# Kernel optimization log

Measured on AMD Instinct MI355X. Metric: run time of the kernel, lower is better.

Reference implementation:

```python
import jax, jax.numpy as jnp
import numpy as np

H, NOPE, ROPE, VD, KV_LORA, HID = 16, 128, 64, 128, 512, 2048
QK = NOPE + ROPE
SCALE = QK ** -0.5
EPS = 1e-5


def _rope(x, freqs):
    # x: [b, t, h, ROPE]; freqs: [t, ROPE//2] angles. Complex-pair rotation.
    cos = jnp.cos(freqs)[None, :, None, :]
    sin = jnp.sin(freqs)[None, :, None, :]
    xr = x.reshape(x.shape[:-1] + (ROPE // 2, 2))
    x1, x2 = xr[..., 0], xr[..., 1]
    o1 = x1 * cos - x2 * sin
    o2 = x1 * sin + x2 * cos
    return jnp.stack([o1, o2], axis=-1).reshape(x.shape)


def _layernorm(x, g, b):
    mu = jnp.mean(x, axis=-1, keepdims=True)
    var = jnp.var(x, axis=-1, keepdims=True)
    return (x - mu) * jax.lax.rsqrt(var + EPS) * g + b


def setup_inputs() -> dict:
    key = jax.random.key(0)
    ks = jax.random.split(key, 6)
    b, t = 2, 2048

    def xavier(k, shape):
        fan_in, fan_out = shape
        lim = np.sqrt(6.0 / (fan_in + fan_out))
        return jax.random.uniform(k, shape, jnp.float32, -lim, lim)

    hidden_states = jax.random.normal(ks[0], (b, t, HID), jnp.float32)
    # rope angles: theta_i = 10000^(-2i/ROPE), angle[p,i] = p * theta_i
    inv_freq = 1.0 / (10000.0 ** (np.arange(0, ROPE, 2, dtype=np.float32) / ROPE))
    freqs = jnp.asarray(np.arange(t, dtype=np.float32)[:, None] * inv_freq[None, :])
    # causal additive mask broadcastable to [b,t,s,h]
    causal = jnp.where(jnp.arange(t)[None, :] <= jnp.arange(t)[:, None], 0.0, -1e9)
    attention_mask = causal.astype(jnp.float32)[None, :, :, None]
    return {
        "hidden_states": hidden_states,
        "freqs": freqs,
        "attention_mask": attention_mask,
        "Wq": xavier(ks[1], (HID, H * QK)),
        "Wkv_a": xavier(ks[2], (HID, KV_LORA + ROPE)),
        "kv_gamma": jnp.ones((KV_LORA,), jnp.float32),
        "kv_beta": jnp.zeros((KV_LORA,), jnp.float32),
        "Wkv_b": xavier(ks[3], (KV_LORA, H * (NOPE + VD))),
        "Wout": xavier(ks[4], (H * VD, HID)),
    }


def reference(hidden_states, freqs, attention_mask, Wq, Wkv_a, kv_gamma, kv_beta, Wkv_b, Wout):
    b, t, _ = hidden_states.shape
    # Q projection -> [b,t,H,QK], split nope/rope, rotate rope part
    q = (hidden_states @ Wq).reshape(b, t, H, QK)
    q_nope, q_rope = q[..., :NOPE], q[..., NOPE:]
    q_rope = _rope(q_rope, freqs)
    # compressed KV latent + shared rope key
    kv = hidden_states @ Wkv_a                      # [b,t,KV_LORA+ROPE]
    kv_lat, k_rope = kv[..., :KV_LORA], kv[..., KV_LORA:]
    k_rope = _rope(k_rope[:, :, None, :], freqs)    # [b,t,1,ROPE]
    kv_lat = _layernorm(kv_lat, kv_gamma, kv_beta)
    kvb = (kv_lat @ Wkv_b).reshape(b, t, H, NOPE + VD)
    k_nope, v = kvb[..., :NOPE], kvb[..., NOPE:]
    k = jnp.concatenate([k_nope, jnp.broadcast_to(k_rope, (b, t, H, ROPE))], axis=-1)
    q = jnp.concatenate([q_nope, q_rope], axis=-1)
    # scores [b,t,s,h]; NOTE: source applies softmax over dim=-1 == HEAD axis (faithful)
    scores = jnp.einsum("bthd,bshd->btsh", q, k) * SCALE + attention_mask
    weights = jax.nn.softmax(scores.astype(jnp.float32), axis=-1).astype(q.dtype)
    attn = jnp.einsum("btsh,bshd->bthd", weights, v).reshape(b, t, H * VD)
    return attn @ Wout
```

## Files before the change

### kernel.cpp

```cpp
#include <hip/hip_runtime.h>

typedef unsigned short u16;
typedef short bf16x8 __attribute__((ext_vector_type(8)));
typedef float f32x4 __attribute__((ext_vector_type(4)));
typedef float f32x16 __attribute__((ext_vector_type(16)));
typedef unsigned short u16x8 __attribute__((ext_vector_type(8)));
typedef unsigned short u16x4 __attribute__((ext_vector_type(4)));

#define GLOBAL_AS __attribute__((address_space(1)))
#define LDS_AS __attribute__((address_space(3)))
#define DEVINL __device__ __forceinline__

#define BATCH 2
#define TSEQ 2048
#define NHEAD 16
#define QK 192
#define VD 128
#define HID 2048
#define MROWS 4096
#define SCALE_QK 0.07216878364870323f

DEVINL float b2f(u16 u) { union { unsigned i; float f; } x; x.i = ((unsigned)u) << 16; return x.f; }
DEVINL u16 f2b(float f) {
    union { float f; unsigned u; } x; x.f = f;
    unsigned r = x.u + 0x7fffu + ((x.u >> 16) & 1u);
    return (u16)(r >> 16);
}
DEVINL void gload_lds16(const u16* g, u16* l) {
    __builtin_amdgcn_global_load_lds((const GLOBAL_AS unsigned*)g, (LDS_AS unsigned*)l, 16, 0, 0);
}
DEVINL unsigned pk2(float a, float b) {
    unsigned d;
    asm("v_cvt_pk_bf16_f32 %0, %1, %2" : "=v"(d) : "v"(a), "v"(b));
    return d;
}


__global__ void cvt_bf16x8(const float* __restrict__ in, u16* __restrict__ out, int n8) {
    int i = blockIdx.x * 256 + threadIdx.x;
    if (i < n8) {
        const float4* p = (const float4*)(in + (size_t)i * 8);
        float4 x = p[0], y = p[1];
        u16x8 o;
        o[0] = f2b(x.x); o[1] = f2b(x.y); o[2] = f2b(x.z); o[3] = f2b(x.w);
        o[4] = f2b(y.x); o[5] = f2b(y.y); o[6] = f2b(y.z); o[7] = f2b(y.w);
        *(u16x8*)(out + (size_t)i * 8) = o;
    }
}

__global__ void rope_tab_k(const float* __restrict__ freqs, float2* __restrict__ tab) {
    int i = blockIdx.x * 256 + threadIdx.x;
    float f = freqs[i], s, c;
    sincosf(f, &s, &c);
    tab[i] = make_float2(c, s);
}

__global__ void transpose_cvt(const float* __restrict__ in, u16* __restrict__ out,
                              int R, int C, int Cpad) {
    __shared__ float tile[32][33];
    int c0 = blockIdx.x * 32, r0 = blockIdx.y * 32;
    int tx = threadIdx.x, ty = threadIdx.y;
#pragma unroll
    for (int j = 0; j < 4; j++) {
        int r = r0 + ty + j * 8, c = c0 + tx;
        tile[ty + j * 8][tx] = (c < C) ? in[(size_t)r * C + c] : 0.f;
    }
    __syncthreads();
#pragma unroll
    for (int j = 0; j < 4; j++) {
        int oc = c0 + ty + j * 8;
        int orr = r0 + tx;
        if (oc < Cpad) out[(size_t)oc * R + orr] = f2b(tile[tx][ty + j * 8]);
    }
}

template<int MODE>
__global__ __launch_bounds__(256)
void gemm_bt(const u16* __restrict__ A, const u16* __restrict__ BT, int Kdim,
             void* __restrict__ out0, void* __restrict__ out1, void* __restrict__ out2,
             const float2* __restrict__ tab) {
    __shared__ __align__(16) u16 As[128 * 32];
    __shared__ __align__(16) u16 Bs[128 * 32];
    const int tid = threadIdx.x, lane = tid & 63, wave = tid >> 6;
    const int m0 = blockIdx.x * 128, n0 = blockIdx.y * 128;
    const int wr = wave >> 1, wc = wave & 1;

    f32x4 acc[4][4];
#pragma unroll
    for (int i = 0; i < 4; i++)
#pragma unroll
        for (int j = 0; j < 4; j++) acc[i][j] = f32x4{0.f, 0.f, 0.f, 0.f};

    const int e0 = (wave * 2 + 0) * 512 + lane * 8;
    const int e1 = (wave * 2 + 1) * 512 + lane * 8;
    const u16* gA0 = A + (size_t)(m0 + (e0 >> 5)) * Kdim + (e0 & 31);
    const u16* gA1 = A + (size_t)(m0 + (e1 >> 5)) * Kdim + (e1 & 31);
    const u16* gB0 = BT + (size_t)(n0 + (e0 >> 5)) * Kdim + (e0 & 31);
    const u16* gB1 = BT + (size_t)(n0 + (e1 >> 5)) * Kdim + (e1 & 31);
    u16* lA0 = &As[(wave * 2 + 0) * 512];
    u16* lA1 = &As[(wave * 2 + 1) * 512];
    u16* lB0 = &Bs[(wave * 2 + 0) * 512];
    u16* lB1 = &Bs[(wave * 2 + 1) * 512];

    const int arow = lane & 15, koff = (lane >> 4) * 8;

    for (int k0 = 0; k0 < Kdim; k0 += 32) {
        gload_lds16(gA0, lA0); gload_lds16(gA1, lA1);
        gload_lds16(gB0, lB0); gload_lds16(gB1, lB1);
        gA0 += 32; gA1 += 32; gB0 += 32; gB1 += 32;
        asm volatile("s_waitcnt vmcnt(0)" ::: "memory");
        __syncthreads();
        bf16x8 af[4], bfr[4];
#pragma unroll
        for (int i = 0; i < 4; i++)
            af[i] = *(const bf16x8*)&As[(wr * 64 + i * 16 + arow) * 32 + koff];
#pragma unroll
        for (int j = 0; j < 4; j++)
            bfr[j] = *(const bf16x8*)&Bs[(wc * 64 + j * 16 + arow) * 32 + koff];
#pragma unroll
        for (int i = 0; i < 4; i++)
#pragma unroll
            for (int j = 0; j < 4; j++)
                acc[i][j] = __builtin_amdgcn_mfma_f32_16x16x32_bf16(af[i], bfr[j], acc[i][j], 0, 0, 0);
        __syncthreads();
    }

#pragma unroll
    for (int i = 0; i < 4; i++)
#pragma unroll
        for (int j = 0; j < 4; j++)
#pragma unroll
            for (int r = 0; r < 4; r++) {
                int row = m0 + wr * 64 + i * 16 + (lane >> 4) * 4 + r;
                int col = n0 + wc * 64 + j * 16 + (lane & 15);
                float v = acc[i][j][r];
                if constexpr (MODE == 0) {
                    int h = col / 192, d = col % 192;
                    int b = row >> 11, t = row & 2047;
                    float vv = v;
                    float pv = __shfl_xor(v, 1);
                    if (d >= 128) {
                        float2 cs = tab[t * 32 + ((d - 128) >> 1)];
                        vv = v * cs.x + pv * ((lane & 1) ? cs.y : -cs.y);
                    }
                    ((u16*)out0)[((size_t)(b * 16 + h) * 2048 + t) * 192 + d] = f2b(vv);
                } else if constexpr (MODE == 1) {
                    ((float*)out0)[(size_t)row * 640 + col] = v;
                } else if constexpr (MODE == 2) {
                    int h = col >> 8, d = col & 255;
                    int b = row >> 11, t = row & 2047;
                    size_t base = (size_t)(b * 16 + h) * 2048 + t;
                    if (d < 128) ((u16*)out0)[base * 192 + d] = f2b(v);
                    else {
                        u16 bv = f2b(v);
                        ((u16*)out1)[base * 128 + (d - 128)] = bv;
                        ((u16*)out2)[((size_t)(b * 16 + h) * 128 + (d - 128)) * 2048 + t] = bv;
                    }
                } else {
                    ((float*)out0)[(size_t)row * 2048 + col] = v;
                }
            }
}

__global__ __launch_bounds__(256)
void ln_krope(const float* __restrict__ kvf, const float* __restrict__ gamma,
              const float* __restrict__ beta, const float2* __restrict__ tab,
              u16* __restrict__ kvlat, u16* __restrict__ kbuf) {
    int row = blockIdx.x, tid = threadIdx.x;
    const float* x = kvf + (size_t)row * 640;
    float v0 = x[tid], v1 = x[tid + 256];
    float s = v0 + v1, sq = v0 * v0 + v1 * v1;
#pragma unroll
    for (int off = 1; off < 64; off <<= 1) { s += __shfl_xor(s, off); sq += __shfl_xor(sq, off); }
    __shared__ float ssum[4], ssq[4];
    if ((tid & 63) == 0) { ssum[tid >> 6] = s; ssq[tid >> 6] = sq; }
    __syncthreads();
    s = ssum[0] + ssum[1] + ssum[2] + ssum[3];
    sq = ssq[0] + ssq[1] + ssq[2] + ssq[3];
    float mu = s * (1.f / 512.f);
    float var = sq * (1.f / 512.f) - mu * mu;
    float rs = rsqrtf(var + 1e-5f);
    kvlat[(size_t)row * 512 + tid] = f2b((v0 - mu) * rs * gamma[tid] + beta[tid]);
    kvlat[(size_t)row * 512 + tid + 256] = f2b((v1 - mu) * rs * gamma[tid + 256] + beta[tid + 256]);
    if (tid < 32) {
        int t = row & 2047, b = row >> 11;
        float x1 = x[512 + 2 * tid], x2 = x[512 + 2 * tid + 1];
        float2 cs = tab[t * 32 + tid];
        u16 u1 = f2b(x1 * cs.x - x2 * cs.y), u2 = f2b(x1 * cs.y + x2 * cs.x);
        for (int h = 0; h < 16; ++h) {
            size_t base = ((size_t)(b * 16 + h) * 2048 + t) * 192 + 128 + 2 * tid;
            kbuf[base] = u1; kbuf[base + 1] = u2;
        }
    }
}

__global__ void suff1(const u16* __restrict__ vbuf, float* __restrict__ psum) {
    int bh = blockIdx.x, c = blockIdx.y, d = threadIdx.x;
    float s = 0.f;
    const u16* vp = vbuf + ((size_t)bh * 2048 + c * 128) * 128 + d;
    for (int tt = 0; tt < 128; ++tt) s += b2f(vp[(size_t)tt * 128]);
    psum[((size_t)bh * 16 + c) * 128 + d] = s;
}
__global__ void suff2(const float* __restrict__ psum, float* __restrict__ csuf) {
    int bh = blockIdx.x, d = threadIdx.x;
    float run = 0.f;
    for (int c = 15; c >= 0; --c) {
        csuf[((size_t)bh * 16 + c) * 128 + d] = run;
        run += psum[((size_t)bh * 16 + c) * 128 + d];
    }
}
__global__ void suff3(const u16* __restrict__ vbuf, const float* __restrict__ csuf,
                      u16* __restrict__ attnb) {
    int bh = blockIdx.x, c = blockIdx.y, d = threadIdx.x;
    int b = bh >> 4, h = bh & 15;
    float run = csuf[((size_t)bh * 16 + c) * 128 + d];
    for (int tt = 127; tt >= 0; --tt) {
        int t = c * 128 + tt;
        attnb[((size_t)b * 2048 + t) * 2048 + h * 128 + d] = f2b(run * 0.0625f);
        run += b2f(vbuf[((size_t)bh * 2048 + t) * 128 + d]);
    }
}

__global__ __launch_bounds__(256, 3)
void z_kernel(const u16* __restrict__ qbuf, const u16* __restrict__ kbuf,
              u16* __restrict__ ztb) {
    __shared__ __align__(16) u16 Ks[2 * 12288];
    const int tid = threadIdx.x, lane = tid & 63, wave = tid >> 6;
    const int hi = lane >> 5, l31 = lane & 31;
    const int tgrp = wave & 1, sblk = wave >> 1;
    int id = blockIdx.x;
    int b = id & 1, p = id >> 1;
    int tT = 0;
    for (;;) { int cnt = (tT + 2) >> 1; if (p < cnt) break; p -= cnt; ++tT; }
    const int g2 = p * 2;
    const int ns = ((tT + 1 - g2) >= 2) ? 2 : 1;
    const int t0 = tT * 64;
    const int rK = sblk * 32 + l31;
    const int t_loc = tgrp * 32 + l31;

    bf16x8 qA[12];
    auto QLOAD = [&](int h) {
        const u16* qp = qbuf + ((size_t)(b * 16 + h) * 2048 + t0 + t_loc) * 192 + hi * 8;
#pragma unroll
        for (int kk = 0; kk < 12; kk++) qA[kk] = *(const bf16x8*)(qp + kk * 16);
    };
    auto KSTAGE = [&](int h, int st, int bi) {
        const size_t hrow = (size_t)(b * 16 + h) * 2048;
        const int s0 = st * 64;
#pragma unroll
        for (int j2 = 0; j2 < 6; j2++) {
            int idx = (wave * 6 + j2) * 64 + lane;
            int rr2 = idx / 24, cc = idx % 24, cs = cc ^ (rr2 & 7);
            gload_lds16(kbuf + (hrow + s0 + rr2) * 192 + cs * 8, &Ks[bi * 12288 + idx * 8]);
        }
    };
    f32x16 za0, za1;
#pragma unroll
    for (int r = 0; r < 16; r++) { za0[r] = 0.f; za1[r] = 0.f; }
    auto COMPUTE = [&](f32x16& za, const u16* K) {
        f32x16 e;
#pragma unroll
        for (int r = 0; r < 16; r++) e[r] = 0.f;
        __builtin_amdgcn_s_setprio(1);
#pragma unroll
        for (int kk = 0; kk < 12; kk++) {
            int slot = (2 * kk + hi) ^ (rK & 7);
            bf16x8 kf = *(const bf16x8*)&K[rK * 192 + slot * 8];
            e = __builtin_amdgcn_mfma_f32_32x32x16_bf16(kf, qA[kk], e, 0, 0, 0);
        }
        __builtin_amdgcn_s_setprio(0);
#pragma unroll
        for (int r = 0; r < 16; r++) za[r] += __expf(e[r] * SCALE_QK);
    };

    QLOAD(0);
    KSTAGE(0, g2, 0);
    asm volatile("s_waitcnt vmcnt(0)" ::: "memory");
    __builtin_amdgcn_s_barrier();
    int kb = 0;
#pragma unroll 1
    for (int h = 0; h < 16; ++h) {
        if (ns == 2)      KSTAGE(h, g2 + 1, kb ^ 1);
        else if (h < 15)  KSTAGE(h + 1, g2, kb ^ 1);
        if (ns == 2 || h < 15) {
            if (h > 0) { asm volatile("s_waitcnt vmcnt(18)" ::: "memory"); }
            else       { asm volatile("s_waitcnt vmcnt(6)"  ::: "memory"); }
        } else {
            asm volatile("s_waitcnt vmcnt(12)" ::: "memory");
        }
        __builtin_amdgcn_s_barrier();
        __builtin_amdgcn_sched_barrier(0);
        COMPUTE(za0, &Ks[kb * 12288]);
        __builtin_amdgcn_s_barrier();
        if (ns == 1 && h < 15) QLOAD(h + 1);
        kb ^= 1;
        if (ns == 2) {
            if (h < 15) {
                KSTAGE(h + 1, g2, kb ^ 1);
                asm volatile("s_waitcnt vmcnt(6)" ::: "memory");
            } else {
                asm volatile("s_waitcnt vmcnt(0)" ::: "memory");
            }
            __builtin_amdgcn_s_barrier();
            __builtin_amdgcn_sched_barrier(0);
            COMPUTE(za1, &Ks[kb * 12288]);
            __builtin_amdgcn_s_barrier();
            if (h < 15) QLOAD(h + 1);
            kb ^= 1;
        }
    }
    const size_t trow = ((size_t)b * 2048 + t0 + t_loc) * 2048;
#pragma unroll
    for (int g3 = 0; g3 < 4; g3++) {
        u16x4 zo;
#pragma unroll
        for (int j = 0; j < 4; j++) zo[j] = f2b(__fdividef(1.f, za0[g3 * 4 + j]));
        *(u16x4*)&ztb[trow + g2 * 64 + sblk * 32 + 4 * hi + 8 * g3] = zo;
    }
    if (ns == 2) {
#pragma unroll
        for (int g3 = 0; g3 < 4; g3++) {
            u16x4 zo;
#pragma unroll
            for (int j = 0; j < 4; j++) zo[j] = f2b(__fdividef(1.f, za1[g3 * 4 + j]));
            *(u16x4*)&ztb[trow + (g2 + 1) * 64 + sblk * 32 + 4 * hi + 8 * g3] = zo;
        }
    }
}

__global__ __launch_bounds__(512, 1)
void attn_pv(const u16* __restrict__ qbuf, const u16* __restrict__ kbuf,
             const u16* __restrict__ vtbuf, const u16* __restrict__ ztb,
             u16* __restrict__ attnb) {
    __shared__ __align__(16) u16 lds[40960];
    u16* Ks = lds;
    u16* Vt = lds + 24576;
    const int tid = threadIdx.x, lane = tid & 63, wave = tid >> 6;
    const int hi = lane >> 5, l31 = lane & 31;
    const int tgrp = wave & 3, sblk = wave >> 2;
    int id = blockIdx.x;
    int xcd = id & 7, j2 = id >> 3;
    int pr = j2 & 7, g = j2 >> 3;
    int bh = xcd * 4 + g;
    const int b = bh >> 4, h = bh & 15;
    const size_t kvrow = (size_t)bh * 2048;
    const int rK = sblk * 32 + l31;
    const int t_loc = tgrp * 32 + l31;

    for (int part = 0; part < 2; ++part) {
        const int T = part ? (15 - pr) : pr;
        const int t0p = T * 128, nst = 2 * T + 2;
        const int tg = t0p + t_loc;
        const u16* zrow = ztb + ((size_t)b * 2048 + tg) * 2048;
        const int zbase0 = sblk * 32 + 4 * hi;

        bf16x8 qf[12];
        {
            const u16* qp = qbuf + (kvrow + tg) * 192 + hi * 8;
#pragma unroll
            for (int kk = 0; kk < 12; kk++) qf[kk] = *(const bf16x8*)(qp + kk * 16);
        }
        f32x16 o[4];
#pragma unroll
        for (int db = 0; db < 4; db++)
#pragma unroll
            for (int r = 0; r < 16; r++) o[db][r] = 0.f;

        auto STAGE = [&](int st, int bi) {
            const int s0 = st * 64;
#pragma unroll
            for (int j = 0; j < 3; j++) {
                int idx = (wave * 3 + j) * 64 + lane;
                int rr2 = idx / 24, cc = idx % 24, cs = cc ^ (rr2 & 7);
                gload_lds16(kbuf + (kvrow + s0 + rr2) * 192 + cs * 8, &Ks[bi * 12288 + idx * 8]);
            }
#pragma unroll
            for (int j = 0; j < 2; j++) {
                int idx = (wave * 2 + j) * 64 + lane;
                int d = idx >> 3, cc = idx & 7, cs = cc ^ (d & 7);
                gload_lds16(vtbuf + ((size_t)bh * 128 + d) * 2048 + s0 + cs * 8, &Vt[bi * 8192 + idx * 8]);
            }
        };
        u16x4 zc0, zc1, zc2, zc3, zn0, zn1, zn2, zn3;
        auto ZLOAD = [&](int st, u16x4& a, u16x4& bb, u16x4& c, u16x4& d) {
            int base = st * 64 + zbase0;
            a  = *(const u16x4*)(zrow + base);
            bb = *(const u16x4*)(zrow + base + 8);
            c  = *(const u16x4*)(zrow + base + 16);
            d  = *(const u16x4*)(zrow + base + 24);
        };
        STAGE(0, 0);
        ZLOAD(0, zc0, zc1, zc2, zc3);
        for (int st = 0; st < nst; ++st) {
            int cur = st & 1;
            if (st + 1 < nst) {
                STAGE(st + 1, cur ^ 1);
                ZLOAD(st + 1, zn0, zn1, zn2, zn3);
                asm volatile("s_waitcnt vmcnt(9)" ::: "memory");
            } else {
                asm volatile("s_waitcnt vmcnt(0)" ::: "memory");
            }
            __builtin_amdgcn_s_barrier();
            __builtin_amdgcn_sched_barrier(0);
            const u16* Kc = &Ks[cur * 12288];
            const u16* Vc = &Vt[cur * 8192];
            f32x16 sacc;
#pragma unroll
            for (int r = 0; r < 16; r++) sacc[r] = 0.f;
            __builtin_amdgcn_s_setprio(1);
#pragma unroll
            for (int kk = 0; kk < 12; kk++) {
                int slot = (2 * kk + hi) ^ (rK & 7);
                bf16x8 kf = *(const bf16x8*)&Kc[rK * 192 + slot * 8];
                sacc = __builtin_amdgcn_mfma_f32_32x32x16_bf16(kf, qf[kk], sacc, 0, 0, 0);
            }
            __builtin_amdgcn_s_setprio(0);
            const int s0g = st * 64 + sblk * 32;
            float w[16];
#define SMG(g3, zcv)                                                        \
_Pragma("unroll")                                                           \
            for (int j = 0; j < 4; j++) {                                   \
                int r = g3 * 4 + j;                                         \
                int spat = j + 8 * g3 + 4 * hi;                             \
                w[r] = (s0g + spat <= tg)                                   \
                     ? __expf(sacc[r] * SCALE_QK) * b2f(zcv[j]) : 0.f;      \
            }
            SMG(0, zc0) SMG(1, zc1) SMG(2, zc2) SMG(3, zc3)
#undef SMG
            unsigned pw0 = pk2(w[0], w[1]), pw1 = pk2(w[2], w[3]);
            unsigned pw2 = pk2(w[4], w[5]), pw3 = pk2(w[6], w[7]);
            unsigned pw4 = pk2(w[8], w[9]), pw5 = pk2(w[10], w[11]);
            unsigned pw6 = pk2(w[12], w[13]), pw7 = pk2(w[14], w[15]);
            unsigned a0 = pw0, a1 = pw1, a2 = pw4, a3 = pw5;
            asm volatile("v_permlane32_swap_b32 %0, %1" : "+v"(a0), "+v"(pw2));
            asm volatile("v_permlane32_swap_b32 %0, %1" : "+v"(a1), "+v"(pw3));
            asm volatile("v_permlane32_swap_b32 %0, %1" : "+v"(a2), "+v"(pw6));
            asm volatile("v_permlane32_swap_b32 %0, %1" : "+v"(a3), "+v"(pw7));
            union PU { unsigned u[4]; bf16x8 v; } p0, p1;
            p0.u[0] = a0;  p0.u[1] = a1;  p0.u[2] = pw2; p0.u[3] = pw3;
            p1.u[0] = a2;  p1.u[1] = a3;  p1.u[2] = pw6; p1.u[3] = pw7;
            __builtin_amdgcn_s_setprio(1);
#pragma unroll
            for (int db = 0; db < 4; db++) {
                int dv = db * 32 + l31;
#pragma unroll
                for (int ks = 0; ks < 2; ks++) {
                    int slot = (sblk * 4 + 2 * ks + hi) ^ (dv & 7);
                    bf16x8 vb = *(const bf16x8*)&Vc[dv * 64 + slot * 8];
                    o[db] = __builtin_amdgcn_mfma_f32_32x32x16_bf16(ks ? p1.v : p0.v, vb, o[db], 0, 0, 0);
                }
            }
            __builtin_amdgcn_s_setprio(0);
            __builtin_amdgcn_s_barrier();
            if (st + 1 < nst) { zc0 = zn0; zc1 = zn1; zc2 = zn2; zc3 = zn3; }
        }
        __syncthreads();
        float* red = (float*)lds;
        if (sblk == 0) {
#pragma unroll
            for (int db = 0; db < 4; db++)
#pragma unroll
                for (int r = 0; r < 16; r++) {
                    int trow = (r & 3) + 8 * (r >> 2) + 4 * hi;
                    red[(tgrp * 32 + trow) * 128 + db * 32 + l31] = o[db][r];
                }
        }
        __syncthreads();
        if (sblk == 1) {
#pragma unroll
            for (int db = 0; db < 4; db++)
#pragma unroll
                for (int r = 0; r < 16; r++) {
                    int trow = (r & 3) + 8 * (r >> 2) + 4 * hi;
                    float val = o[db][r] + red[(tgrp * 32 + trow) * 128 + db * 32 + l31];
                    size_t oi = ((size_t)b * 2048 + t0p + tgrp * 32 + trow) * 2048 + h * 128 + db * 32 + l31;
                    attnb[oi] = f2b(val + b2f(attnb[oi]));
                }
        }
        __syncthreads();
    }
}

extern "C" void kernel_launch(void* const* d_in, const int* in_sizes, int n_in,
                              void* d_out, int out_size, void* d_ws, size_t ws_size,
                              hipStream_t stream) {
    (void)in_sizes; (void)n_in; (void)out_size;
    const float* hidden = (const float*)d_in[0];
    const float* freqs  = (const float*)d_in[1];
    const float* Wq     = (const float*)d_in[3];
    const float* Wkva   = (const float*)d_in[4];
    const float* gamma  = (const float*)d_in[5];
    const float* beta   = (const float*)d_in[6];
    const float* Wkvb   = (const float*)d_in[7];
    const float* Wout   = (const float*)d_in[8];
    float* outp = (float*)d_out;

    char* ws = (char*)d_ws;
    size_t off = 0;
    auto alloc = [&](size_t bytes) -> void* {
        void* p = ws + off; off += (bytes + 255) & ~(size_t)255; return p;
    };
    u16*   hid_b = (u16*)alloc((size_t)MROWS * HID * 2);
    u16*   WqT   = (u16*)alloc((size_t)3072 * 2048 * 2);
    u16*   WkvaT = (u16*)alloc((size_t)640 * 2048 * 2);
    u16*   WkvbT = (u16*)alloc((size_t)4096 * 512 * 2);
    u16*   WoutT = (u16*)alloc((size_t)2048 * 2048 * 2);
    u16*   qbuf  = (u16*)alloc((size_t)BATCH * NHEAD * TSEQ * QK * 2);
    float* kvf   = (float*)alloc((size_t)MROWS * 640 * 4);
    u16*   kvlat = (u16*)alloc((size_t)MROWS * 512 * 2);
    u16*   kbuf  = (u16*)alloc((size_t)BATCH * NHEAD * TSEQ * QK * 2);
    u16*   vbuf  = (u16*)alloc((size_t)BATCH * NHEAD * TSEQ * VD * 2);
    u16*   attnb = (u16*)alloc((size_t)MROWS * 2048 * 2);
    float2* ropetab = (float2*)alloc((size_t)2048 * 32 * 8);
    float* psum  = (float*)alloc((size_t)32 * 16 * 128 * 4);
    float* csuf  = (float*)alloc((size_t)32 * 16 * 128 * 4);
    if (off > ws_size) return;
    u16* ztb   = WqT;
    u16* vtbuf = hid_b;

    cvt_bf16x8<<<4096, 256, 0, stream>>>(hidden, hid_b, MROWS * HID / 8);
    rope_tab_k<<<256, 256, 0, stream>>>(freqs, ropetab);
    dim3 tb(32, 8);
    transpose_cvt<<<dim3(96, 64), tb, 0, stream>>>(Wq, WqT, 2048, 3072, 3072);
    transpose_cvt<<<dim3(20, 64), tb, 0, stream>>>(Wkva, WkvaT, 2048, 576, 640);
    transpose_cvt<<<dim3(128, 16), tb, 0, stream>>>(Wkvb, WkvbT, 512, 4096, 4096);
    transpose_cvt<<<dim3(64, 64), tb, 0, stream>>>(Wout, WoutT, 2048, 2048, 2048);

    gemm_bt<1><<<dim3(32, 5), 256, 0, stream>>>(hid_b, WkvaT, 2048, kvf, nullptr, nullptr, nullptr);
    gemm_bt<0><<<dim3(32, 24), 256, 0, stream>>>(hid_b, WqT, 2048, qbuf, nullptr, nullptr, ropetab);
    ln_krope<<<MROWS, 256, 0, stream>>>(kvf, gamma, beta, ropetab, kvlat, kbuf);
    gemm_bt<2><<<dim3(32, 32), 256, 0, stream>>>(kvlat, WkvbT, 512, kbuf, vbuf, vtbuf, nullptr);

    suff1<<<dim3(32, 16), 128, 0, stream>>>(vbuf, psum);
    suff2<<<32, 128, 0, stream>>>(psum, csuf);
    suff3<<<dim3(32, 16), 128, 0, stream>>>(vbuf, csuf, attnb);

    z_kernel<<<544, 256, 0, stream>>>(qbuf, kbuf, ztb);
    attn_pv<<<256, 512, 0, stream>>>(qbuf, kbuf, vtbuf, ztb, attnb);

    gemm_bt<3><<<dim3(32, 16), 256, 0, stream>>>(attnb, WoutT, 2048, outp, nullptr, nullptr, nullptr);
}
```

Baseline: 493.0 us.

## Add 256x256 eight-wave pipelined GEMM for Q, KV-b and output projections

Introduces a new GEMM kernel with 256x256 tiles, 8 waves, double-buffered direct-to-LDS loads with XOR swizzle, and staged prefetch interleaved across four MFMA phases with setprio. The Q, KV-b and output projections switch to it, while the old kernel keeps only the KV-a path. The goal is more data reuse per tile and better overlap of global loads with MFMA work. The cost is fewer blocks (e.g. 128 for Wout), 128 KB of LDS per block and heavy register use, which may limit occupancy and wave count on the device.

```diff
diff --git a/kernel.cpp b/kernel.cpp
--- a/kernel.cpp
+++ b/kernel.cpp
@@ -134,6 +134,112 @@
                 int row = m0 + wr * 64 + i * 16 + (lane >> 4) * 4 + r;
                 int col = n0 + wc * 64 + j * 16 + (lane & 15);
                 float v = acc[i][j][r];
+                if constexpr (MODE == 1) {
+                    ((float*)out0)[(size_t)row * 640 + col] = v;
+                }
+                (void)out1; (void)out2; (void)tab;
+            }
+}
+
+template<int MODE>
+__global__ __launch_bounds__(512, 2)
+void gemm8(const u16* __restrict__ A, const u16* __restrict__ BT, int Kdim,
+           void* __restrict__ out0, void* __restrict__ out1, void* __restrict__ out2,
+           const float2* __restrict__ tab) {
+    __shared__ __align__(16) u16 lds[65536];
+    u16* As = lds;
+    u16* Bs = lds + 32768;
+    const int tid = threadIdx.x, lane = tid & 63, wave = tid >> 6;
+    const int wm = wave >> 2, wn = wave & 3;
+    const int m0 = blockIdx.x * 256, n0 = blockIdx.y * 256;
+    const int NK = Kdim >> 6;
+    const int fr = lane & 15, fk = lane >> 4;
+
+    f32x4 acc[8][4];
+#pragma unroll
+    for (int i = 0; i < 8; i++)
+#pragma unroll
+        for (int j = 0; j < 4; j++) acc[i][j] = f32x4{0.f, 0.f, 0.f, 0.f};
+
+    const int srow = tid >> 3;
+    const int skc  = (tid & 7) ^ (srow & 7);
+    const int soff = tid * 8;
+    auto PIECE = [&](const u16* base, int grow0, int k0, u16* ldst) {
+        gload_lds16(base + (size_t)(grow0 + srow) * Kdim + k0 + skc * 8, ldst + soff);
+    };
+    auto STAGE6 = [&](int i) {
+        int bb = i & 1, k0 = i << 6;
+        PIECE(BT, n0 + 0,   k0, Bs + (bb * 2 + 0) * 8192 + 0);
+        PIECE(BT, n0 + 64,  k0, Bs + (bb * 2 + 0) * 8192 + 4096);
+        PIECE(BT, n0 + 128, k0, Bs + (bb * 2 + 1) * 8192 + 0);
+        PIECE(BT, n0 + 192, k0, Bs + (bb * 2 + 1) * 8192 + 4096);
+        PIECE(A,  m0 + 0,   k0, As + (bb * 2 + 0) * 8192 + 0);
+        PIECE(A,  m0 + 128, k0, As + (bb * 2 + 1) * 8192 + 0);
+    };
+    auto STAGE_A0HI = [&](int i) { int bb = i & 1; PIECE(A, m0 + 64,  i << 6, As + (bb * 2 + 0) * 8192 + 4096); };
+    auto STAGE_A1HI = [&](int i) { int bb = i & 1; PIECE(A, m0 + 192, i << 6, As + (bb * 2 + 1) * 8192 + 4096); };
+
+    auto PHASE = [&](int bb, int qr, int qc) {
+        const u16* Ab = As + (bb * 2 + wm) * 8192;
+        const u16* Bb = Bs + (bb * 2 + (wn >> 1)) * 8192;
+        const int bbase = (wn & 1) * 64 + qc * 32;
+        bf16x8 af[2][4], bfv[2][2];
+#pragma unroll
+        for (int kk = 0; kk < 2; kk++) {
+#pragma unroll
+            for (int ii = 0; ii < 4; ii++) {
+                int ar = qr * 64 + ii * 16 + fr;
+                af[kk][ii] = *(const bf16x8*)&Ab[ar * 64 + (((kk * 4 + fk) ^ (ar & 7)) * 8)];
+            }
+#pragma unroll
+            for (int jj = 0; jj < 2; jj++) {
+                int br = bbase + jj * 16 + fr;
+                bfv[kk][jj] = *(const bf16x8*)&Bb[br * 64 + (((kk * 4 + fk) ^ (br & 7)) * 8)];
+            }
+        }
+        __builtin_amdgcn_s_setprio(1);
+#pragma unroll
+        for (int kk = 0; kk < 2; kk++)
+#pragma unroll
+            for (int ii = 0; ii < 4; ii++)
+#pragma unroll
+                for (int jj = 0; jj < 2; jj++)
+                    acc[qr * 4 + ii][qc * 2 + jj] =
+                        __builtin_amdgcn_mfma_f32_16x16x32_bf16(af[kk][ii], bfv[kk][jj],
+                                                                acc[qr * 4 + ii][qc * 2 + jj], 0, 0, 0);
+        __builtin_amdgcn_s_setprio(0);
+    };
+
+    STAGE6(0); STAGE_A0HI(0); STAGE_A1HI(0);
+#pragma unroll 1
+    for (int i = 0; i < NK; ++i) {
+        const int bb = i & 1;
+        const bool more = (i + 1 < NK);
+        asm volatile("s_waitcnt vmcnt(2)" ::: "memory");
+        __builtin_amdgcn_s_barrier();
+        if (more) STAGE6(i + 1);
+        PHASE(bb, 0, 0);
+        __builtin_amdgcn_s_barrier();
+        if (more) STAGE_A0HI(i + 1);
+        PHASE(bb, 0, 1);
+        if (more) { asm volatile("s_waitcnt vmcnt(7)" ::: "memory"); }
+        else      { asm volatile("s_waitcnt vmcnt(0)" ::: "memory"); }
+        __builtin_amdgcn_s_barrier();
+        if (more) STAGE_A1HI(i + 1);
+        PHASE(bb, 1, 0);
+        __builtin_amdgcn_s_barrier();
+        PHASE(bb, 1, 1);
+    }
+
+#pragma unroll
+    for (int ii = 0; ii < 8; ii++)
+#pragma unroll
+        for (int jj = 0; jj < 4; jj++)
+#pragma unroll
+            for (int r = 0; r < 4; r++) {
+                int row = m0 + wm * 128 + ii * 16 + fk * 4 + r;
+                int col = n0 + wn * 64 + jj * 16 + fr;
+                float v = acc[ii][jj][r];
                 if constexpr (MODE == 0) {
                     int h = col / 192, d = col % 192;
                     int b = row >> 11, t = row & 2047;
@@ -144,8 +250,6 @@
                         vv = v * cs.x + pv * ((lane & 1) ? cs.y : -cs.y);
                     }
                     ((u16*)out0)[((size_t)(b * 16 + h) * 2048 + t) * 192 + d] = f2b(vv);
-                } else if constexpr (MODE == 1) {
-                    ((float*)out0)[(size_t)row * 640 + col] = v;
                 } else if constexpr (MODE == 2) {
                     int h = col >> 8, d = col & 255;
                     int b = row >> 11, t = row & 2047;
@@ -527,9 +631,9 @@
     transpose_cvt<<<dim3(64, 64), tb, 0, stream>>>(Wout, WoutT, 2048, 2048, 2048);
 
     gemm_bt<1><<<dim3(32, 5), 256, 0, stream>>>(hid_b, WkvaT, 2048, kvf, nullptr, nullptr, nullptr);
-    gemm_bt<0><<<dim3(32, 24), 256, 0, stream>>>(hid_b, WqT, 2048, qbuf, nullptr, nullptr, ropetab);
+    gemm8<0><<<dim3(16, 12), 512, 0, stream>>>(hid_b, WqT, 2048, qbuf, nullptr, nullptr, ropetab);
     ln_krope<<<MROWS, 256, 0, stream>>>(kvf, gamma, beta, ropetab, kvlat, kbuf);
-    gemm_bt<2><<<dim3(32, 32), 256, 0, stream>>>(kvlat, WkvbT, 512, kbuf, vbuf, vtbuf, nullptr);
+    gemm8<2><<<dim3(16, 16), 512, 0, stream>>>(kvlat, WkvbT, 512, kbuf, vbuf, vtbuf, nullptr);
 
     suff1<<<dim3(32, 16), 128, 0, stream>>>(vbuf, psum);
     suff2<<<32, 128, 0, stream>>>(psum, csuf);
@@ -538,5 +642,5 @@
     z_kernel<<<544, 256, 0, stream>>>(qbuf, kbuf, ztb);
     attn_pv<<<256, 512, 0, stream>>>(qbuf, kbuf, vtbuf, ztb, attnb);
 
-    gemm_bt<3><<<dim3(32, 16), 256, 0, stream>>>(attnb, WoutT, 2048, outp, nullptr, nullptr, nullptr);
-}
+    gemm8<3><<<dim3(16, 8), 512, 0, stream>>>(attnb, WoutT, 2048, outp, nullptr, nullptr, nullptr);
+}
```

Result: no change. 501.5 us (+1.7%).
